# Optimization experiments

Hardware: AMD Instinct MI355X
Metric: run time of the kernel (lower is better)

The kernel has to match this reference:

```python
import jax, jax.numpy as jnp
import numpy as np

E, D_IN, H, D_OUT = 8, 6, 32, 2
B = 1048576

def setup_inputs() -> dict:
    key = jax.random.key(0)
    ks = jax.random.split(key, 11)
    s = lambda *sh: 1.0 / np.sqrt(sh[-2])  # glorot-ish scale
    x = jax.random.normal(ks[0], (B, D_IN), dtype=jnp.float32)
    # stacked expert weights
    W1 = jax.random.normal(ks[1], (E, D_IN, H), dtype=jnp.float32) * (1.0/np.sqrt(D_IN))
    b1 = jnp.zeros((E, H), dtype=jnp.float32)
    W2 = jax.random.normal(ks[2], (E, H, H), dtype=jnp.float32) * (1.0/np.sqrt(H))
    b2 = jnp.zeros((E, H), dtype=jnp.float32)
    W3 = jax.random.normal(ks[3], (E, H, D_OUT), dtype=jnp.float32) * (1.0/np.sqrt(H))
    b3 = jnp.zeros((E, D_OUT), dtype=jnp.float32)
    # gating network
    Wg1 = jax.random.normal(ks[4], (D_IN, H), dtype=jnp.float32) * (1.0/np.sqrt(D_IN))
    bg1 = jnp.zeros((H,), dtype=jnp.float32)
    Wg2 = jax.random.normal(ks[5], (H, E), dtype=jnp.float32) * (1.0/np.sqrt(H))
    bg2 = jnp.zeros((E,), dtype=jnp.float32)
    return {"x": x, "W1": W1, "b1": b1, "W2": W2, "b2": b2, "W3": W3, "b3": b3,
            "Wg1": Wg1, "bg1": bg1, "Wg2": Wg2, "bg2": bg2}

def reference(x, W1, b1, W2, b2, W3, b3, Wg1, bg1, Wg2, bg2):
    # gate: [B, E] softmax probs
    g = jax.nn.softmax(jax.nn.relu(x @ Wg1 + bg1) @ Wg2 + bg2, axis=-1)
    # all experts as batched GEMMs: h1, h2 [B, E, H]; y [B, E, 2]
    h1 = jax.nn.relu(jnp.einsum('bd,edh->beh', x, W1) + b1)
    h2 = jax.nn.relu(jnp.einsum('beh,ehk->bek', h1, W2) + b2)
    y = jnp.einsum('beh,eho->beo', h2, W3) + b3
    # gate-weighted sum over experts -> [B, 2]
    return jnp.einsum('be,beo->bo', g, y)
```

## Files before the change

kernel.cpp:

```cpp
#include <hip/hip_runtime.h>


typedef _Float16 half2_t __attribute__((ext_vector_type(2)));
typedef _Float16 half8_t __attribute__((ext_vector_type(8)));
typedef __fp16   fp16v2  __attribute__((ext_vector_type(2)));
typedef float  f32x16   __attribute__((ext_vector_type(16)));
typedef float  float4_t __attribute__((ext_vector_type(4)));
typedef float  float2_t __attribute__((ext_vector_type(2)));
typedef int    int4_t   __attribute__((ext_vector_type(4)));

#define MFMA32(A, B, C) __builtin_amdgcn_mfma_f32_32x32x16_f16((A), (B), (C), 0, 0, 0)

static constexpr int E_ = 8, DIN_ = 6, H_ = 32;

union H8U { half2_t h2[4]; half8_t h8; int4_t i4; };
union HI  { half2_t h; int i; };
union PKU { fp16v2 p; half2_t h; };
union C16 { f32x16 v; float4_t q[4]; };

__device__ __forceinline__ half2_t pkrtz(float a, float b) {
    PKU u; u.p = __builtin_amdgcn_cvt_pkrtz(a, b);
    return u.h;
}

__device__ __forceinline__ half2_t relu2(half2_t v) {
    const half2_t z = {(_Float16)0.0f, (_Float16)0.0f};
    return __builtin_elementwise_max(v, z);
}

__global__ __launch_bounds__(256)
__attribute__((amdgpu_waves_per_eu(3, 3)))
void moe_kernel(
    const float* __restrict__ x,  const float* __restrict__ W1, const float* __restrict__ b1,
    const float* __restrict__ W2, const float* __restrict__ b2, const float* __restrict__ W3,
    const float* __restrict__ b3, const float* __restrict__ Wg1, const float* __restrict__ bg1,
    const float* __restrict__ Wg2, const float* __restrict__ bg2,
    float* __restrict__ out, int nTok, int nTiles, int tilesPerWave)
{
    const int tid  = threadIdx.x;
    const int lane = tid & 63;
    const int m    = lane & 31;
    const int h    = lane >> 5;
    const int wv   = tid >> 6;
    const int gw   = (blockIdx.x << 2) + wv;

    __shared__ H8U w1img[E_][64];
    __shared__ H8U w2img[E_][2][64];
    __shared__ H8U a3img[E_][2][64];
    __shared__ __align__(16) float b2s[E_][H_];
    __shared__ H8U g1s[64];
    __shared__ H8U g2s[2][64];
    __shared__ __align__(16) float b3s[16];
    __shared__ __align__(16) float bg2s[8];

    const float L2E = 1.44269504f;
    const half2_t h2z = pkrtz(0.f, 0.f);

    #pragma unroll
    for (int j = 0; j < 2; ++j) {
        const int e = wv * 2 + j;
        H8U w1v;
        if (h == 0) {
            w1v.h2[0] = pkrtz(W1[(e*DIN_+0)*H_+m], W1[(e*DIN_+1)*H_+m]);
            w1v.h2[1] = pkrtz(W1[(e*DIN_+2)*H_+m], W1[(e*DIN_+3)*H_+m]);
        } else {
            w1v.h2[0] = pkrtz(W1[(e*DIN_+4)*H_+m], W1[(e*DIN_+5)*H_+m]);
            w1v.h2[1] = pkrtz(b1[e*H_+m], 0.f);
        }
        w1v.h2[2] = h2z; w1v.h2[3] = h2z;
        w1img[e][lane] = w1v;

        const int o = m & 1;
        const bool alive = ((m >> 1) == e);
        #pragma unroll
        for (int b = 0; b < 2; ++b) {
            H8U w2v, a3v;
            #pragma unroll
            for (int p = 0; p < 4; ++p) {
                const int k0 = 16*b + 8*(p>>1) + 4*h + 2*(p&1);
                w2v.h2[p] = pkrtz(W2[(e*H_+k0)*H_+m], W2[(e*H_+k0+1)*H_+m]);
                a3v.h2[p] = alive ? pkrtz(W3[(e*H_+k0)*2+o], W3[(e*H_+k0+1)*2+o]) : h2z;
            }
            w2img[e][b][lane] = w2v;
            a3img[e][b][lane] = a3v;
        }
        if (lane < H_) b2s[e][lane] = b2[e*H_ + lane];
    }

    if (wv == 0) {
        H8U g1v;
        if (h == 0) {
            g1v.h2[0] = pkrtz(Wg1[0*H_+m], Wg1[1*H_+m]);
            g1v.h2[1] = pkrtz(Wg1[2*H_+m], Wg1[3*H_+m]);
        } else {
            g1v.h2[0] = pkrtz(Wg1[4*H_+m], Wg1[5*H_+m]);
            g1v.h2[1] = pkrtz(bg1[m], 0.f);
        }
        g1v.h2[2] = h2z; g1v.h2[3] = h2z;
        g1s[lane] = g1v;

        const bool alive = (m < E_);
        #pragma unroll
        for (int b = 0; b < 2; ++b) {
            H8U g2v;
            #pragma unroll
            for (int p = 0; p < 4; ++p) {
                const int k0 = 16*b + 8*(p>>1) + 4*h + 2*(p&1);
                g2v.h2[p] = alive ? pkrtz(Wg2[k0*E_+m]*L2E, Wg2[(k0+1)*E_+m]*L2E) : h2z;
            }
            g2s[b][lane] = g2v;
        }
        if (lane < 16) b3s[lane] = b3[lane];
        if (lane < E_) bg2s[lane] = bg2[lane] * L2E;
    }

    const f32x16 z16 = {0,0,0,0, 0,0,0,0, 0,0,0,0, 0,0,0,0};
    const float4_t z4 = {0.f, 0.f, 0.f, 0.f};

    __syncthreads();

    const int tile0 = gw * tilesPerWave;
    const int xo1 = h ? 4 : 0;
    const int xo2 = h ? 4 : 2;
    const float* xq = x + ((size_t)tile0 * 32 + m) * DIN_;
    float2_t la = {0.f, 0.f}, lb = {0.f, 0.f};
    if (tile0 < nTiles && (size_t)tile0 * 32 + m < (size_t)nTok) {
        la = *(const float2_t*)(xq + xo1);
        lb = *(const float2_t*)(xq + xo2);
    }
    HI onei; onei.h = pkrtz(1.f, 0.f);

    for (int it = 0; it < tilesPerWave; ++it) {
        const int tile = tile0 + it;
        if (tile >= nTiles) break;
        const bool tok = ((size_t)tile * 32 + m) < (size_t)nTok;

        H8U g1v;  g1v.i4  = *(const volatile int4_t*)&g1s[lane].i4;
        H8U g2v0; g2v0.i4 = *(const volatile int4_t*)&g2s[0][lane].i4;
        H8U g2v1; g2v1.i4 = *(const volatile int4_t*)&g2s[1][lane].i4;
        float4_t bgq  = *(const volatile float4_t*)&bg2s[4*h];
        float4_t b3q0 = *(const volatile float4_t*)&b3s[4*h];
        float4_t b3q1 = *(const volatile float4_t*)&b3s[8 + 4*h];

        H8U xB;
        xB.h2[0] = pkrtz(la[0], la[1]);
        { HI hb; hb.h = pkrtz(lb[0], lb[1]); HI se; se.i = h ? onei.i : hb.i; xB.h2[1] = se.h; }
        xB.h2[2] = h2z; xB.h2[3] = h2z;

        if (it + 1 < tilesPerWave && tile + 1 < nTiles) {
            const float* xn = xq + (size_t)(it + 1) * 32 * DIN_;
            if ((size_t)(tile + 1) * 32 + m < (size_t)nTok) {
                la = *(const float2_t*)(xn + xo1);
                lb = *(const float2_t*)(xn + xo2);
            }
        }

        f32x16 hg = MFMA32(g1v.h8, xB.h8, z16);
        H8U uhlo, uhhi;
        #pragma unroll
        for (int i = 0; i < 4; ++i) {
            uhlo.h2[i] = relu2(pkrtz(hg[2*i],   hg[2*i+1]));
            uhhi.h2[i] = relu2(pkrtz(hg[8+2*i], hg[8+2*i+1]));
        }
        C16 gc; gc.q[0] = bgq; gc.q[1] = z4; gc.q[2] = z4; gc.q[3] = z4;
        f32x16 gl = MFMA32(g2v0.h8, uhlo.h8, gc.v);
        gl = MFMA32(g2v1.h8, uhhi.h8, gl);

        float ex0 = __builtin_amdgcn_exp2f(gl[0]);
        float ex1 = __builtin_amdgcn_exp2f(gl[1]);
        float ex2 = __builtin_amdgcn_exp2f(gl[2]);
        float ex3 = __builtin_amdgcn_exp2f(gl[3]);
        float s = (ex0 + ex1) + (ex2 + ex3);
        s += __shfl_xor(s, 32);
        float rs = __builtin_amdgcn_rcpf(s);
        float sA = h ? ex0 : ex2, sB = h ? ex1 : ex3;
        HI sp; sp.h = pkrtz(sA, sB);
        HI rp; rp.i = __shfl_xor(sp.i, 32);
        float rA = (float)rp.h[0], rB = (float)rp.h[1];
        float wA = h ? rA : ex0, wB = h ? rB : ex1;
        float wC = h ? ex2 : rA, wD = h ? ex3 : rB;

        f32x16 Y;
        { C16 yc; yc.q[0] = b3q0; yc.q[1] = b3q1; yc.q[2] = z4; yc.q[3] = z4; Y = yc.v; }
        #pragma unroll
        for (int e = 0; e < E_; ++e) {
            H8U a1;   a1.i4   = w1img[e][lane].i4;
            H8U a2lo; a2lo.i4 = w2img[e][0][lane].i4;
            H8U a2hi; a2hi.i4 = w2img[e][1][lane].i4;
            H8U a3lo; a3lo.i4 = a3img[e][0][lane].i4;
            H8U a3hi; a3hi.i4 = a3img[e][1][lane].i4;
            C16 bc;
            bc.q[0] = *(const float4_t*)&b2s[e][4*h];
            bc.q[1] = *(const float4_t*)&b2s[e][8 + 4*h];
            bc.q[2] = *(const float4_t*)&b2s[e][16 + 4*h];
            bc.q[3] = *(const float4_t*)&b2s[e][24 + 4*h];

            f32x16 c1 = MFMA32(a1.h8, xB.h8, z16);
            H8U u1lo, u1hi;
            #pragma unroll
            for (int i = 0; i < 4; ++i) {
                u1lo.h2[i] = relu2(pkrtz(c1[2*i],   c1[2*i+1]));
                u1hi.h2[i] = relu2(pkrtz(c1[8+2*i], c1[8+2*i+1]));
            }
            f32x16 c2 = MFMA32(a2lo.h8, u1lo.h8, bc.v);
            c2 = MFMA32(a2hi.h8, u1hi.h8, c2);
            H8U u2lo, u2hi;
            #pragma unroll
            for (int i = 0; i < 4; ++i) {
                u2lo.h2[i] = relu2(pkrtz(c2[2*i],   c2[2*i+1]));
                u2hi.h2[i] = relu2(pkrtz(c2[8+2*i], c2[8+2*i+1]));
            }
            Y = MFMA32(a3lo.h8, u2lo.h8, Y);
            Y = MFMA32(a3hi.h8, u2hi.h8, Y);
        }

        float p0 = wA*Y[0] + wB*Y[2] + wC*Y[4] + wD*Y[6];
        float p1 = wA*Y[1] + wB*Y[3] + wC*Y[5] + wD*Y[7];
        p0 += __shfl_xor(p0, 32);
        p1 += __shfl_xor(p1, 32);
        if (h == 0 && tok) {
            float2_t ov = {p0 * rs, p1 * rs};
            *(float2_t*)(out + ((size_t)tile * 32 + m) * 2) = ov;
        }
    }
}

extern "C" void kernel_launch(void* const* d_in, const int* in_sizes, int n_in,
                              void* d_out, int out_size, void* d_ws, size_t ws_size,
                              hipStream_t stream) {
    const float* x   = (const float*)d_in[0];
    const float* W1  = (const float*)d_in[1];
    const float* b1  = (const float*)d_in[2];
    const float* W2  = (const float*)d_in[3];
    const float* b2  = (const float*)d_in[4];
    const float* W3  = (const float*)d_in[5];
    const float* b3  = (const float*)d_in[6];
    const float* Wg1 = (const float*)d_in[7];
    const float* bg1 = (const float*)d_in[8];
    const float* Wg2 = (const float*)d_in[9];
    const float* bg2 = (const float*)d_in[10];
    float* out = (float*)d_out;

    const int B      = in_sizes[0] / DIN_;
    const int nTiles = (B + 31) / 32;
    const int blocks = 768;
    const int wavesTotal = blocks * 4;
    const int tpw = (nTiles + wavesTotal - 1) / wavesTotal;

    moe_kernel<<<blocks, 256, 0, stream>>>(x, W1, b1, W2, b2, W3, b3,
                                           Wg1, bg1, Wg2, bg2, out, B, nTiles, tpw);
}
```

Measured before the change: 131.2 us.

## Interleave expert MLP chains in groups of four for MFMA ILP

Processes experts in two batches of four so the independent MFMA chains of different experts interleave, hiding MFMA dependency latency. The output accumulator is split into two chains, and the layer-2 bias moves from the MFMA accumulator init to an fp16 packed add after conversion. Occupancy drops to 2 waves/EU and the grid shrinks to 512 blocks to make room for the extra registers. The fp16 bias add slightly changes rounding.

```diff
diff --git a/kernel.cpp b/kernel.cpp
--- a/kernel.cpp
+++ b/kernel.cpp
@@ -11,7 +11,7 @@
 
 #define MFMA32(A, B, C) __builtin_amdgcn_mfma_f32_32x32x16_f16((A), (B), (C), 0, 0, 0)
 
-static constexpr int E_ = 8, DIN_ = 6, H_ = 32;
+static constexpr int E_ = 8, DIN_ = 6, H_ = 32, EB_ = 4;
 
 union H8U { half2_t h2[4]; half8_t h8; int4_t i4; };
 union HI  { half2_t h; int i; };
@@ -29,7 +29,7 @@
 }
 
 __global__ __launch_bounds__(256)
-__attribute__((amdgpu_waves_per_eu(3, 3)))
+__attribute__((amdgpu_waves_per_eu(2, 2)))
 void moe_kernel(
     const float* __restrict__ x,  const float* __restrict__ W1, const float* __restrict__ b1,
     const float* __restrict__ W2, const float* __restrict__ b2, const float* __restrict__ W3,
@@ -47,7 +47,7 @@
     __shared__ H8U w1img[E_][64];
     __shared__ H8U w2img[E_][2][64];
     __shared__ H8U a3img[E_][2][64];
-    __shared__ __align__(16) float b2s[E_][H_];
+    __shared__ int4_t b2pk[E_][2][2];
     __shared__ H8U g1s[64];
     __shared__ H8U g2s[2][64];
     __shared__ __align__(16) float b3s[16];
@@ -84,7 +84,17 @@
             w2img[e][b][lane] = w2v;
             a3img[e][b][lane] = a3v;
         }
-        if (lane < H_) b2s[e][lane] = b2[e*H_ + lane];
+        H8U b2lo, b2hi;
+        #pragma unroll
+        for (int p = 0; p < 4; ++p) {
+            const int r0 = 2*p, r1 = 2*p + 1;
+            const int rr0 = (r0&3) + 8*(r0>>2) + 4*h;
+            const int rr1 = (r1&3) + 8*(r1>>2) + 4*h;
+            b2lo.h2[p] = pkrtz(b2[e*H_ + rr0],      b2[e*H_ + rr1]);
+            b2hi.h2[p] = pkrtz(b2[e*H_ + 16 + rr0], b2[e*H_ + 16 + rr1]);
+        }
+        b2pk[e][h][0] = b2lo.i4;
+        b2pk[e][h][1] = b2hi.i4;
     }
 
     if (wv == 0) {
@@ -180,42 +190,74 @@
         float wA = h ? rA : ex0, wB = h ? rB : ex1;
         float wC = h ? ex2 : rA, wD = h ? ex3 : rB;
 
-        f32x16 Y;
-        { C16 yc; yc.q[0] = b3q0; yc.q[1] = b3q1; yc.q[2] = z4; yc.q[3] = z4; Y = yc.v; }
-        #pragma unroll
-        for (int e = 0; e < E_; ++e) {
-            H8U a1;   a1.i4   = w1img[e][lane].i4;
-            H8U a2lo; a2lo.i4 = w2img[e][0][lane].i4;
-            H8U a2hi; a2hi.i4 = w2img[e][1][lane].i4;
-            H8U a3lo; a3lo.i4 = a3img[e][0][lane].i4;
-            H8U a3hi; a3hi.i4 = a3img[e][1][lane].i4;
-            C16 bc;
-            bc.q[0] = *(const float4_t*)&b2s[e][4*h];
-            bc.q[1] = *(const float4_t*)&b2s[e][8 + 4*h];
-            bc.q[2] = *(const float4_t*)&b2s[e][16 + 4*h];
-            bc.q[3] = *(const float4_t*)&b2s[e][24 + 4*h];
-
-            f32x16 c1 = MFMA32(a1.h8, xB.h8, z16);
-            H8U u1lo, u1hi;
-            #pragma unroll
-            for (int i = 0; i < 4; ++i) {
-                u1lo.h2[i] = relu2(pkrtz(c1[2*i],   c1[2*i+1]));
-                u1hi.h2[i] = relu2(pkrtz(c1[8+2*i], c1[8+2*i+1]));
-            }
-            f32x16 c2 = MFMA32(a2lo.h8, u1lo.h8, bc.v);
-            c2 = MFMA32(a2hi.h8, u1hi.h8, c2);
-            H8U u2lo, u2hi;
-            #pragma unroll
-            for (int i = 0; i < 4; ++i) {
-                u2lo.h2[i] = relu2(pkrtz(c2[2*i],   c2[2*i+1]));
-                u2hi.h2[i] = relu2(pkrtz(c2[8+2*i], c2[8+2*i+1]));
-            }
-            Y = MFMA32(a3lo.h8, u2lo.h8, Y);
-            Y = MFMA32(a3hi.h8, u2hi.h8, Y);
-        }
-
-        float p0 = wA*Y[0] + wB*Y[2] + wC*Y[4] + wD*Y[6];
-        float p1 = wA*Y[1] + wB*Y[3] + wC*Y[5] + wD*Y[7];
+        f32x16 Ya, Yb;
+        { C16 yc; yc.q[0] = b3q0; yc.q[1] = b3q1; yc.q[2] = z4; yc.q[3] = z4; Ya = yc.v; }
+        Yb = z16;
+        #pragma unroll
+        for (int bb = 0; bb < 2; ++bb) {
+            const int eb = bb * EB_;
+
+            H8U a1[EB_];
+            #pragma unroll
+            for (int j = 0; j < EB_; ++j) a1[j].i4 = w1img[eb + j][lane].i4;
+            f32x16 c1[EB_];
+            #pragma unroll
+            for (int j = 0; j < EB_; ++j) c1[j] = MFMA32(a1[j].h8, xB.h8, z16);
+
+            H8U a2lo[EB_], a2hi[EB_];
+            #pragma unroll
+            for (int j = 0; j < EB_; ++j) {
+                a2lo[j].i4 = w2img[eb + j][0][lane].i4;
+                a2hi[j].i4 = w2img[eb + j][1][lane].i4;
+            }
+
+            H8U u1lo[EB_], u1hi[EB_];
+            #pragma unroll
+            for (int j = 0; j < EB_; ++j)
+                #pragma unroll
+                for (int i = 0; i < 4; ++i) {
+                    u1lo[j].h2[i] = relu2(pkrtz(c1[j][2*i],   c1[j][2*i+1]));
+                    u1hi[j].h2[i] = relu2(pkrtz(c1[j][8+2*i], c1[j][8+2*i+1]));
+                }
+
+            f32x16 c2[EB_];
+            #pragma unroll
+            for (int j = 0; j < EB_; ++j) c2[j] = MFMA32(a2lo[j].h8, u1lo[j].h8, z16);
+            #pragma unroll
+            for (int j = 0; j < EB_; ++j) c2[j] = MFMA32(a2hi[j].h8, u1hi[j].h8, c2[j]);
+
+            H8U b2l[EB_], b2h[EB_], a3lo[EB_], a3hi[EB_];
+            #pragma unroll
+            for (int j = 0; j < EB_; ++j) {
+                b2l[j].i4  = *(const int4_t*)&b2pk[eb + j][h][0];
+                b2h[j].i4  = *(const int4_t*)&b2pk[eb + j][h][1];
+                a3lo[j].i4 = a3img[eb + j][0][lane].i4;
+                a3hi[j].i4 = a3img[eb + j][1][lane].i4;
+            }
+
+            H8U u2lo[EB_], u2hi[EB_];
+            #pragma unroll
+            for (int j = 0; j < EB_; ++j)
+                #pragma unroll
+                for (int i = 0; i < 4; ++i) {
+                    u2lo[j].h2[i] = relu2(pkrtz(c2[j][2*i],   c2[j][2*i+1])   + b2l[j].h2[i]);
+                    u2hi[j].h2[i] = relu2(pkrtz(c2[j][8+2*i], c2[j][8+2*i+1]) + b2h[j].h2[i]);
+                }
+
+            #pragma unroll
+            for (int j = 0; j < EB_; ++j) {
+                if (j & 1) {
+                    Yb = MFMA32(a3lo[j].h8, u2lo[j].h8, Yb);
+                    Yb = MFMA32(a3hi[j].h8, u2hi[j].h8, Yb);
+                } else {
+                    Ya = MFMA32(a3lo[j].h8, u2lo[j].h8, Ya);
+                    Ya = MFMA32(a3hi[j].h8, u2hi[j].h8, Ya);
+                }
+            }
+        }
+
+        float p0 = wA*(Ya[0]+Yb[0]) + wB*(Ya[2]+Yb[2]) + wC*(Ya[4]+Yb[4]) + wD*(Ya[6]+Yb[6]);
+        float p1 = wA*(Ya[1]+Yb[1]) + wB*(Ya[3]+Yb[3]) + wC*(Ya[5]+Yb[5]) + wD*(Ya[7]+Yb[7]);
         p0 += __shfl_xor(p0, 32);
         p1 += __shfl_xor(p1, 32);
         if (h == 0 && tok) {
@@ -243,7 +285,7 @@
 
     const int B      = in_sizes[0] / DIN_;
     const int nTiles = (B + 31) / 32;
-    const int blocks = 768;
+    const int blocks = 512;
     const int wavesTotal = blocks * 4;
     const int tpw = (nTiles + wavesTotal - 1) / wavesTotal;
 
```

Result: slower. 134.7 us (+2.7%).
